# Performance work log

Measured on AMD Instinct MI355X. Metric: run time of the kernel, lower is better.

The kernel has to match this reference:

```python
import jax, jax.numpy as jnp
import numpy as np

DIM_CODES = 512
DICT_SIZE = 512
EMBED_DIM = 16
BATCH = 512


def setup_inputs() -> dict:
    key = jax.random.key(0)
    k1, k2 = jax.random.split(key)
    mu = jax.random.normal(k1, (BATCH, DIM_CODES * EMBED_DIM), dtype=jnp.float32)
    dictionary = jax.random.normal(k2, (DIM_CODES, DICT_SIZE, EMBED_DIM), dtype=jnp.float32)
    return {"mu": mu, "dictionary": dictionary}


def reference(mu, dictionary):
    # mu: [B, C*E], dictionary: [C, K, E]
    B = mu.shape[0]
    C, K, E = dictionary.shape
    mu3 = mu.reshape(B, C, E)
    # pairwise squared distance ||mu - d||^2 = ||mu||^2 + ||d||^2 - 2 mu.d -> [B, C, K]
    dist = (jnp.sum(mu3 * mu3, axis=-1)[..., None]
            + jnp.sum(dictionary * dictionary, axis=-1)[None]
            - 2.0 * jnp.einsum('bce,cke->bck', mu3, dictionary))
    idx = jnp.argmin(dist, axis=-1)  # [B, C] int
    # gather nearest codebook entries: per-code index into its own codebook
    z_embed = dictionary[jnp.arange(C)[None, :], idx]  # [B, C, E]
    z_embed = z_embed.reshape(B, C * E)
    # TransferGrad: forward = z_embed, backward passes grad straight-through to mu
    z = mu + jax.lax.stop_gradient(z_embed - mu)
    one_hot_idx = jax.nn.one_hot(idx, K, dtype=mu.dtype)  # [B, C, K]
    return z, z_embed, one_hot_idx
```

## Files before the change

kernel.cpp:

```cpp
#include <hip/hip_runtime.h>
#include <float.h>

constexpr int C    = 512;
constexpr int K    = 512;
constexpr int E    = 16;
constexpr int B    = 512;
constexpr int ROWS = 128;
constexpr int MUS  = C * E;

__launch_bounds__(256, 2)
__global__ void vq_kernel(const float* __restrict__ mu,
                          const float* __restrict__ dict,
                          float* __restrict__ z,
                          float* __restrict__ zq,
                          float* __restrict__ oh)
{
    const int c    = blockIdx.x;
    const int b0   = blockIdx.y * ROWS;
    const int tid  = threadIdx.x;
    const int lane = tid & 63;
    const int wave = tid >> 6;

    __shared__ float mu_s[ROWS][E];

    const float* __restrict__ dbase = dict + (size_t)c * K * E;

    float4 dv[8][4];
    float  nrm[8];
#pragma unroll
    for (int i = 0; i < 8; ++i) {
        const int k = lane + 64 * i;
        const float4* p = reinterpret_cast<const float4*>(dbase + k * E);
        dv[i][0] = p[0]; dv[i][1] = p[1]; dv[i][2] = p[2]; dv[i][3] = p[3];
        float s = dv[i][0].x * dv[i][0].x;
        s = fmaf(dv[i][0].y, dv[i][0].y, s);
        s = fmaf(dv[i][0].z, dv[i][0].z, s);
        s = fmaf(dv[i][0].w, dv[i][0].w, s);
#pragma unroll
        for (int t = 1; t < 4; ++t) {
            s = fmaf(dv[i][t].x, dv[i][t].x, s);
            s = fmaf(dv[i][t].y, dv[i][t].y, s);
            s = fmaf(dv[i][t].z, dv[i][t].z, s);
            s = fmaf(dv[i][t].w, dv[i][t].w, s);
        }
        nrm[i] = s;
    }

    {
        const int r = tid >> 2, q = tid & 3;
#pragma unroll
        for (int rep = 0; rep < 2; ++rep) {
            const int row = r + rep * 64;
            const float4* p = reinterpret_cast<const float4*>(
                mu + (size_t)(b0 + row) * MUS + c * E);
            reinterpret_cast<float4*>(&mu_s[row][0])[q] = p[q];
        }
    }
    __syncthreads();

    for (int j = 0; j < ROWS / 4; ++j) {
        const int bl = wave + 4 * j;
        const int b  = b0 + bl;

        float4 m[4];
#pragma unroll
        for (int t = 0; t < 4; ++t)
            m[t] = reinterpret_cast<const float4*>(&mu_s[bl][0])[t];

        float nmu = m[0].x * m[0].x;
        nmu = fmaf(m[0].y, m[0].y, nmu);
        nmu = fmaf(m[0].z, m[0].z, nmu);
        nmu = fmaf(m[0].w, m[0].w, nmu);
#pragma unroll
        for (int t = 1; t < 4; ++t) {
            nmu = fmaf(m[t].x, m[t].x, nmu);
            nmu = fmaf(m[t].y, m[t].y, nmu);
            nmu = fmaf(m[t].z, m[t].z, nmu);
            nmu = fmaf(m[t].w, m[t].w, nmu);
        }

        float dist_v[8];
        float best_d = FLT_MAX;
        int   best_k = K;
#pragma unroll
        for (int i = 0; i < 8; ++i) {
            float acc = dv[i][0].x * m[0].x;
            acc = fmaf(dv[i][0].y, m[0].y, acc);
            acc = fmaf(dv[i][0].z, m[0].z, acc);
            acc = fmaf(dv[i][0].w, m[0].w, acc);
#pragma unroll
            for (int t = 1; t < 4; ++t) {
                acc = fmaf(dv[i][t].x, m[t].x, acc);
                acc = fmaf(dv[i][t].y, m[t].y, acc);
                acc = fmaf(dv[i][t].z, m[t].z, acc);
                acc = fmaf(dv[i][t].w, m[t].w, acc);
            }
            const float dist = fmaf(-2.0f, acc, nmu + nrm[i]);
            dist_v[i] = dist;
            const int k = lane + 64 * i;
            if (dist < best_d) { best_d = dist; best_k = k; }
        }

#pragma unroll
        for (int off = 32; off; off >>= 1) {
            const float od = __shfl_down(best_d, off);
            const int   ok = __shfl_down(best_k, off);
            if (od < best_d || (od == best_d && ok < best_k)) {
                best_d = od; best_k = ok;
            }
        }
        best_k = __shfl(best_k, 0);
        best_d = __shfl(best_d, 0);

        float sec = FLT_MAX;
#pragma unroll
        for (int i = 0; i < 8; ++i) {
            const int k = lane + 64 * i;
            sec = (k != best_k) ? fminf(sec, dist_v[i]) : sec;
        }
#pragma unroll
        for (int off = 32; off; off >>= 1)
            sec = fminf(sec, __shfl_down(sec, off));
        sec = __shfl(sec, 0);

        if (sec - best_d < 1e-3f) {
            double nmuD = 0.0;
#pragma unroll
            for (int t = 0; t < 4; ++t) {
                nmuD += (double)m[t].x * m[t].x + (double)m[t].y * m[t].y
                      + (double)m[t].z * m[t].z + (double)m[t].w * m[t].w;
            }
            double bd = DBL_MAX;
            int    bk = K;
#pragma unroll
            for (int i = 0; i < 8; ++i) {
                double nd = 0.0, dt = 0.0;
#pragma unroll
                for (int t = 0; t < 4; ++t) {
                    nd += (double)dv[i][t].x * dv[i][t].x
                        + (double)dv[i][t].y * dv[i][t].y
                        + (double)dv[i][t].z * dv[i][t].z
                        + (double)dv[i][t].w * dv[i][t].w;
                    dt += (double)dv[i][t].x * m[t].x
                        + (double)dv[i][t].y * m[t].y
                        + (double)dv[i][t].z * m[t].z
                        + (double)dv[i][t].w * m[t].w;
                }
                const double dist = nmuD + nd - 2.0 * dt;
                const int k = lane + 64 * i;
                if (dist < bd) { bd = dist; bk = k; }
            }
#pragma unroll
            for (int off = 32; off; off >>= 1) {
                const double od = __shfl_down(bd, off);
                const int    ok = __shfl_down(bk, off);
                if (od < bd || (od == bd && ok < bk)) { bd = od; bk = ok; }
            }
            best_k = __shfl(bk, 0);
        }

        float* ohp = oh + ((size_t)b * C + c) * K;
#pragma unroll
        for (int h = 0; h < 2; ++h) {
            const int kb = h * 256 + lane * 4;
            float4 v;
            v.x = (kb + 0 == best_k) ? 1.0f : 0.0f;
            v.y = (kb + 1 == best_k) ? 1.0f : 0.0f;
            v.z = (kb + 2 == best_k) ? 1.0f : 0.0f;
            v.w = (kb + 3 == best_k) ? 1.0f : 0.0f;
            *reinterpret_cast<float4*>(ohp + kb) = v;
        }

        if (lane < E) {
            const float dq = dbase[best_k * E + lane];
            const float mm = mu_s[bl][lane];
            const size_t o = (size_t)b * MUS + (size_t)c * E + lane;
            zq[o] = dq;
            z[o]  = mm + (dq - mm);
        }
    }
}

extern "C" void kernel_launch(void* const* d_in, const int* in_sizes, int n_in,
                              void* d_out, int out_size, void* d_ws, size_t ws_size,
                              hipStream_t stream)
{
    const float* mu   = (const float*)d_in[0];
    const float* dict = (const float*)d_in[1];

    float* z  = (float*)d_out;
    float* zq = z  + (size_t)B * C * E;
    float* oh = zq + (size_t)B * C * E;

    dim3 grid(C, B / ROWS);
    vq_kernel<<<grid, 256, 0, stream>>>(mu, dict, z, zq, oh);
}
```

Baseline: 695.7 us.

## Batch four rows per wave with packed argmin reduction and single-pass second-min

```diff
diff --git a/kernel.cpp b/kernel.cpp
--- a/kernel.cpp
+++ b/kernel.cpp
@@ -58,123 +58,153 @@
     }
     __syncthreads();
 
-    for (int j = 0; j < ROWS / 4; ++j) {
-        const int bl = wave + 4 * j;
-        const int b  = b0 + bl;
-
-        float4 m[4];
-#pragma unroll
-        for (int t = 0; t < 4; ++t)
-            m[t] = reinterpret_cast<const float4*>(&mu_s[bl][0])[t];
-
-        float nmu = m[0].x * m[0].x;
-        nmu = fmaf(m[0].y, m[0].y, nmu);
-        nmu = fmaf(m[0].z, m[0].z, nmu);
-        nmu = fmaf(m[0].w, m[0].w, nmu);
-#pragma unroll
-        for (int t = 1; t < 4; ++t) {
-            nmu = fmaf(m[t].x, m[t].x, nmu);
-            nmu = fmaf(m[t].y, m[t].y, nmu);
-            nmu = fmaf(m[t].z, m[t].z, nmu);
-            nmu = fmaf(m[t].w, m[t].w, nmu);
-        }
-
-        float dist_v[8];
-        float best_d = FLT_MAX;
-        int   best_k = K;
-#pragma unroll
-        for (int i = 0; i < 8; ++i) {
-            float acc = dv[i][0].x * m[0].x;
-            acc = fmaf(dv[i][0].y, m[0].y, acc);
-            acc = fmaf(dv[i][0].z, m[0].z, acc);
-            acc = fmaf(dv[i][0].w, m[0].w, acc);
+    for (int j = 0; j < ROWS / 16; ++j) {
+        unsigned long long pk[4];
+        float              sec[4];
+
+#pragma unroll
+        for (int r = 0; r < 4; ++r) {
+            const int bl = wave + 16 * j + 4 * r;
+
+            float4 m[4];
+#pragma unroll
+            for (int t = 0; t < 4; ++t)
+                m[t] = reinterpret_cast<const float4*>(&mu_s[bl][0])[t];
+
+            float nmu = m[0].x * m[0].x;
+            nmu = fmaf(m[0].y, m[0].y, nmu);
+            nmu = fmaf(m[0].z, m[0].z, nmu);
+            nmu = fmaf(m[0].w, m[0].w, nmu);
 #pragma unroll
             for (int t = 1; t < 4; ++t) {
-                acc = fmaf(dv[i][t].x, m[t].x, acc);
-                acc = fmaf(dv[i][t].y, m[t].y, acc);
-                acc = fmaf(dv[i][t].z, m[t].z, acc);
-                acc = fmaf(dv[i][t].w, m[t].w, acc);
-            }
-            const float dist = fmaf(-2.0f, acc, nmu + nrm[i]);
-            dist_v[i] = dist;
-            const int k = lane + 64 * i;
-            if (dist < best_d) { best_d = dist; best_k = k; }
+                nmu = fmaf(m[t].x, m[t].x, nmu);
+                nmu = fmaf(m[t].y, m[t].y, nmu);
+                nmu = fmaf(m[t].z, m[t].z, nmu);
+                nmu = fmaf(m[t].w, m[t].w, nmu);
+            }
+
+            float best_d = FLT_MAX;
+            int   best_k = K;
+            float sc     = FLT_MAX;
+#pragma unroll
+            for (int i = 0; i < 8; ++i) {
+                float acc = dv[i][0].x * m[0].x;
+                acc = fmaf(dv[i][0].y, m[0].y, acc);
+                acc = fmaf(dv[i][0].z, m[0].z, acc);
+                acc = fmaf(dv[i][0].w, m[0].w, acc);
+#pragma unroll
+                for (int t = 1; t < 4; ++t) {
+                    acc = fmaf(dv[i][t].x, m[t].x, acc);
+                    acc = fmaf(dv[i][t].y, m[t].y, acc);
+                    acc = fmaf(dv[i][t].z, m[t].z, acc);
+                    acc = fmaf(dv[i][t].w, m[t].w, acc);
+                }
+                const float dist = fmaf(-2.0f, acc, nmu + nrm[i]);
+                sc = fminf(sc, fmaxf(best_d, dist));
+                if (dist < best_d) { best_d = dist; best_k = lane + 64 * i; }
+            }
+            pk[r]  = ((unsigned long long)__float_as_uint(best_d) << 32)
+                   | (unsigned)best_k;
+            sec[r] = sc;
         }
 
 #pragma unroll
         for (int off = 32; off; off >>= 1) {
-            const float od = __shfl_down(best_d, off);
-            const int   ok = __shfl_down(best_k, off);
-            if (od < best_d || (od == best_d && ok < best_k)) {
-                best_d = od; best_k = ok;
-            }
-        }
-        best_k = __shfl(best_k, 0);
-        best_d = __shfl(best_d, 0);
-
-        float sec = FLT_MAX;
-#pragma unroll
-        for (int i = 0; i < 8; ++i) {
-            const int k = lane + 64 * i;
-            sec = (k != best_k) ? fminf(sec, dist_v[i]) : sec;
-        }
-#pragma unroll
-        for (int off = 32; off; off >>= 1)
-            sec = fminf(sec, __shfl_down(sec, off));
-        sec = __shfl(sec, 0);
-
-        if (sec - best_d < 1e-3f) {
-            double nmuD = 0.0;
-#pragma unroll
-            for (int t = 0; t < 4; ++t) {
-                nmuD += (double)m[t].x * m[t].x + (double)m[t].y * m[t].y
-                      + (double)m[t].z * m[t].z + (double)m[t].w * m[t].w;
-            }
-            double bd = DBL_MAX;
-            int    bk = K;
-#pragma unroll
-            for (int i = 0; i < 8; ++i) {
-                double nd = 0.0, dt = 0.0;
+            unsigned long long opk[4];
+            float              osec[4];
+#pragma unroll
+            for (int r = 0; r < 4; ++r) {
+                opk[r]  = __shfl_down(pk[r], off);
+                osec[r] = __shfl_down(sec[r], off);
+            }
+#pragma unroll
+            for (int r = 0; r < 4; ++r) {
+                const float a  = __uint_as_float((unsigned)(pk[r]  >> 32));
+                const float b2 = __uint_as_float((unsigned)(opk[r] >> 32));
+                sec[r] = fminf(fminf(sec[r], osec[r]), fmaxf(a, b2));
+                if (opk[r] < pk[r]) pk[r] = opk[r];
+            }
+        }
+
+        int bk0 = 0, bk1 = 0, bk2 = 0, bk3 = 0;
+#pragma unroll
+        for (int r = 0; r < 4; ++r) {
+            const int klo = __builtin_amdgcn_readfirstlane((int)(unsigned)pk[r]);
+            const int dhi = __builtin_amdgcn_readfirstlane((int)(pk[r] >> 32));
+            const int shi = __builtin_amdgcn_readfirstlane(__float_as_int(sec[r]));
+            int  bkr = klo;
+            const float bd = __int_as_float(dhi);
+            const float sc = __int_as_float(shi);
+
+            if (sc - bd < 1e-3f) {
+                const int bl = wave + 16 * j + 4 * r;
+                float4 m[4];
+#pragma unroll
+                for (int t = 0; t < 4; ++t)
+                    m[t] = reinterpret_cast<const float4*>(&mu_s[bl][0])[t];
+                double nmuD = 0.0;
 #pragma unroll
                 for (int t = 0; t < 4; ++t) {
-                    nd += (double)dv[i][t].x * dv[i][t].x
-                        + (double)dv[i][t].y * dv[i][t].y
-                        + (double)dv[i][t].z * dv[i][t].z
-                        + (double)dv[i][t].w * dv[i][t].w;
-                    dt += (double)dv[i][t].x * m[t].x
-                        + (double)dv[i][t].y * m[t].y
-                        + (double)dv[i][t].z * m[t].z
-                        + (double)dv[i][t].w * m[t].w;
-                }
-                const double dist = nmuD + nd - 2.0 * dt;
-                const int k = lane + 64 * i;
-                if (dist < bd) { bd = dist; bk = k; }
-            }
-#pragma unroll
-            for (int off = 32; off; off >>= 1) {
-                const double od = __shfl_down(bd, off);
-                const int    ok = __shfl_down(bk, off);
-                if (od < bd || (od == bd && ok < bk)) { bd = od; bk = ok; }
-            }
-            best_k = __shfl(bk, 0);
-        }
-
-        float* ohp = oh + ((size_t)b * C + c) * K;
-#pragma unroll
-        for (int h = 0; h < 2; ++h) {
-            const int kb = h * 256 + lane * 4;
-            float4 v;
-            v.x = (kb + 0 == best_k) ? 1.0f : 0.0f;
-            v.y = (kb + 1 == best_k) ? 1.0f : 0.0f;
-            v.z = (kb + 2 == best_k) ? 1.0f : 0.0f;
-            v.w = (kb + 3 == best_k) ? 1.0f : 0.0f;
-            *reinterpret_cast<float4*>(ohp + kb) = v;
-        }
-
-        if (lane < E) {
-            const float dq = dbase[best_k * E + lane];
-            const float mm = mu_s[bl][lane];
-            const size_t o = (size_t)b * MUS + (size_t)c * E + lane;
+                    nmuD += (double)m[t].x * m[t].x + (double)m[t].y * m[t].y
+                          + (double)m[t].z * m[t].z + (double)m[t].w * m[t].w;
+                }
+                double bdd = DBL_MAX;
+                int    bkk = K;
+#pragma unroll
+                for (int i = 0; i < 8; ++i) {
+                    double nd = 0.0, dt = 0.0;
+#pragma unroll
+                    for (int t = 0; t < 4; ++t) {
+                        nd += (double)dv[i][t].x * dv[i][t].x
+                            + (double)dv[i][t].y * dv[i][t].y
+                            + (double)dv[i][t].z * dv[i][t].z
+                            + (double)dv[i][t].w * dv[i][t].w;
+                        dt += (double)dv[i][t].x * m[t].x
+                            + (double)dv[i][t].y * m[t].y
+                            + (double)dv[i][t].z * m[t].z
+                            + (double)dv[i][t].w * m[t].w;
+                    }
+                    const double dist = nmuD + nd - 2.0 * dt;
+                    const int k = lane + 64 * i;
+                    if (dist < bdd) { bdd = dist; bkk = k; }
+                }
+#pragma unroll
+                for (int off = 32; off; off >>= 1) {
+                    const double od = __shfl_down(bdd, off);
+                    const int    ok = __shfl_down(bkk, off);
+                    if (od < bdd || (od == bdd && ok < bkk)) { bdd = od; bkk = ok; }
+                }
+                bkr = __builtin_amdgcn_readfirstlane(bkk);
+            }
+
+            if (r == 0) bk0 = bkr; else if (r == 1) bk1 = bkr;
+            else if (r == 2) bk2 = bkr; else bk3 = bkr;
+
+            const int bl = wave + 16 * j + 4 * r;
+            float* ohp = oh + ((size_t)(b0 + bl) * C + c) * K;
+#pragma unroll
+            for (int h = 0; h < 2; ++h) {
+                const int kb = h * 256 + lane * 4;
+                float4 v;
+                v.x = (kb + 0 == bkr) ? 1.0f : 0.0f;
+                v.y = (kb + 1 == bkr) ? 1.0f : 0.0f;
+                v.z = (kb + 2 == bkr) ? 1.0f : 0.0f;
+                v.w = (kb + 3 == bkr) ? 1.0f : 0.0f;
+                *reinterpret_cast<float4*>(ohp + kb) = v;
+            }
+        }
+
+        {
+            const int r = lane >> 4;
+            const int e = lane & 15;
+            int bkr = bk0;
+            bkr = (r == 1) ? bk1 : bkr;
+            bkr = (r == 2) ? bk2 : bkr;
+            bkr = (r == 3) ? bk3 : bkr;
+            const int bl = wave + 16 * j + 4 * r;
+            const float dq = dbase[bkr * E + e];
+            const float mm = mu_s[bl][e];
+            const size_t o = (size_t)(b0 + bl) * MUS + (size_t)c * E + e;
             zq[o] = dq;
             z[o]  = mm + (dq - mm);
         }
```

Result: slower. 1.098 ms (+57.8%).

## Batch four rows per wave iteration with packed 64-bit argmin reductions

Applied to the files above, without the earlier changes.

```diff
diff --git a/kernel.cpp b/kernel.cpp
--- a/kernel.cpp
+++ b/kernel.cpp
@@ -8,7 +8,23 @@
 constexpr int ROWS = 128;
 constexpr int MUS  = C * E;
 
-__launch_bounds__(256, 2)
+__device__ __forceinline__ float fdot4(const float4 a, const float4 b, float acc) {
+    acc = fmaf(a.x, b.x, acc);
+    acc = fmaf(a.y, b.y, acc);
+    acc = fmaf(a.z, b.z, acc);
+    acc = fmaf(a.w, b.w, acc);
+    return acc;
+}
+__device__ __forceinline__ double ddot4(const float4 a, const float4 b, double acc) {
+    return acc + ((double)a.x * b.x + (double)a.y * b.y
+                + (double)a.z * b.z + (double)a.w * b.w);
+}
+__device__ __forceinline__ double dnrm4(const float4 a, double acc) {
+    return acc + ((double)a.x * a.x + (double)a.y * a.y
+                + (double)a.z * a.z + (double)a.w * a.w);
+}
+
+__launch_bounds__(256, 1)
 __global__ void vq_kernel(const float* __restrict__ mu,
                           const float* __restrict__ dict,
                           float* __restrict__ z,
@@ -25,26 +41,23 @@
 
     const float* __restrict__ dbase = dict + (size_t)c * K * E;
 
-    float4 dv[8][4];
-    float  nrm[8];
-#pragma unroll
-    for (int i = 0; i < 8; ++i) {
-        const int k = lane + 64 * i;
-        const float4* p = reinterpret_cast<const float4*>(dbase + k * E);
-        dv[i][0] = p[0]; dv[i][1] = p[1]; dv[i][2] = p[2]; dv[i][3] = p[3];
-        float s = dv[i][0].x * dv[i][0].x;
-        s = fmaf(dv[i][0].y, dv[i][0].y, s);
-        s = fmaf(dv[i][0].z, dv[i][0].z, s);
-        s = fmaf(dv[i][0].w, dv[i][0].w, s);
-#pragma unroll
-        for (int t = 1; t < 4; ++t) {
-            s = fmaf(dv[i][t].x, dv[i][t].x, s);
-            s = fmaf(dv[i][t].y, dv[i][t].y, s);
-            s = fmaf(dv[i][t].z, dv[i][t].z, s);
-            s = fmaf(dv[i][t].w, dv[i][t].w, s);
-        }
-        nrm[i] = s;
-    }
+#define FOR8(X) X(0) X(1) X(2) X(3) X(4) X(5) X(6) X(7)
+
+#define DECL_D(i) float4 d##i##_0, d##i##_1, d##i##_2, d##i##_3; float n##i;
+    FOR8(DECL_D)
+#undef DECL_D
+
+#define LOAD_D(i) { \
+    const float4* p = reinterpret_cast<const float4*>( \
+        dbase + (size_t)(lane + 64 * i) * E); \
+    d##i##_0 = p[0]; d##i##_1 = p[1]; d##i##_2 = p[2]; d##i##_3 = p[3]; \
+    float s = fdot4(d##i##_0, d##i##_0, 0.0f); \
+    s = fdot4(d##i##_1, d##i##_1, s); \
+    s = fdot4(d##i##_2, d##i##_2, s); \
+    s = fdot4(d##i##_3, d##i##_3, s); \
+    n##i = s; }
+    FOR8(LOAD_D)
+#undef LOAD_D
 
     {
         const int r = tid >> 2, q = tid & 3;
@@ -58,127 +71,122 @@
     }
     __syncthreads();
 
-    for (int j = 0; j < ROWS / 4; ++j) {
-        const int bl = wave + 4 * j;
-        const int b  = b0 + bl;
-
-        float4 m[4];
-#pragma unroll
-        for (int t = 0; t < 4; ++t)
-            m[t] = reinterpret_cast<const float4*>(&mu_s[bl][0])[t];
-
-        float nmu = m[0].x * m[0].x;
-        nmu = fmaf(m[0].y, m[0].y, nmu);
-        nmu = fmaf(m[0].z, m[0].z, nmu);
-        nmu = fmaf(m[0].w, m[0].w, nmu);
-#pragma unroll
-        for (int t = 1; t < 4; ++t) {
-            nmu = fmaf(m[t].x, m[t].x, nmu);
-            nmu = fmaf(m[t].y, m[t].y, nmu);
-            nmu = fmaf(m[t].z, m[t].z, nmu);
-            nmu = fmaf(m[t].w, m[t].w, nmu);
-        }
-
-        float dist_v[8];
-        float best_d = FLT_MAX;
-        int   best_k = K;
-#pragma unroll
-        for (int i = 0; i < 8; ++i) {
-            float acc = dv[i][0].x * m[0].x;
-            acc = fmaf(dv[i][0].y, m[0].y, acc);
-            acc = fmaf(dv[i][0].z, m[0].z, acc);
-            acc = fmaf(dv[i][0].w, m[0].w, acc);
-#pragma unroll
-            for (int t = 1; t < 4; ++t) {
-                acc = fmaf(dv[i][t].x, m[t].x, acc);
-                acc = fmaf(dv[i][t].y, m[t].y, acc);
-                acc = fmaf(dv[i][t].z, m[t].z, acc);
-                acc = fmaf(dv[i][t].w, m[t].w, acc);
-            }
-            const float dist = fmaf(-2.0f, acc, nmu + nrm[i]);
-            dist_v[i] = dist;
-            const int k = lane + 64 * i;
-            if (dist < best_d) { best_d = dist; best_k = k; }
-        }
+#pragma unroll 1
+    for (int j = 0; j < ROWS / 16; ++j) {
+        unsigned long long pk0, pk1, pk2, pk3;
+        float sec0, sec1, sec2, sec3;
+
+#define DIST1(i) { \
+    float acc = fdot4(d##i##_0, m0, 0.0f); \
+    acc = fdot4(d##i##_1, m1, acc); \
+    acc = fdot4(d##i##_2, m2, acc); \
+    acc = fdot4(d##i##_3, m3, acc); \
+    const float dist = fmaf(-2.0f, acc, nmu + n##i); \
+    sc = fminf(sc, fmaxf(best_d, dist)); \
+    if (dist < best_d) { best_d = dist; best_k = lane + 64 * i; } }
+
+#define PHASE1(r) { \
+    const int bl = wave + 16 * j + 4 * r; \
+    const float4* mp = reinterpret_cast<const float4*>(&mu_s[bl][0]); \
+    const float4 m0 = mp[0], m1 = mp[1], m2 = mp[2], m3 = mp[3]; \
+    float nmu = fdot4(m0, m0, 0.0f); \
+    nmu = fdot4(m1, m1, nmu); \
+    nmu = fdot4(m2, m2, nmu); \
+    nmu = fdot4(m3, m3, nmu); \
+    float best_d = FLT_MAX; \
+    int   best_k = K; \
+    float sc     = FLT_MAX; \
+    FOR8(DIST1) \
+    pk##r = ((unsigned long long)__float_as_uint(best_d) << 32) \
+          | (unsigned)best_k; \
+    sec##r = sc; }
+
+        PHASE1(0) PHASE1(1) PHASE1(2) PHASE1(3)
+#undef PHASE1
+#undef DIST1
 
 #pragma unroll
         for (int off = 32; off; off >>= 1) {
-            const float od = __shfl_down(best_d, off);
-            const int   ok = __shfl_down(best_k, off);
-            if (od < best_d || (od == best_d && ok < best_k)) {
-                best_d = od; best_k = ok;
-            }
+#define SHUF(r) { \
+            const unsigned long long o  = __shfl_down(pk##r, off); \
+            const float              os = __shfl_down(sec##r, off); \
+            const float ax = __uint_as_float((unsigned)(pk##r >> 32)); \
+            const float bx = __uint_as_float((unsigned)(o     >> 32)); \
+            sec##r = fminf(fminf(sec##r, os), fmaxf(ax, bx)); \
+            if (o < pk##r) pk##r = o; }
+            SHUF(0) SHUF(1) SHUF(2) SHUF(3)
+#undef SHUF
         }
-        best_k = __shfl(best_k, 0);
-        best_d = __shfl(best_d, 0);
-
-        float sec = FLT_MAX;
-#pragma unroll
-        for (int i = 0; i < 8; ++i) {
-            const int k = lane + 64 * i;
-            sec = (k != best_k) ? fminf(sec, dist_v[i]) : sec;
-        }
-#pragma unroll
-        for (int off = 32; off; off >>= 1)
-            sec = fminf(sec, __shfl_down(sec, off));
-        sec = __shfl(sec, 0);
-
-        if (sec - best_d < 1e-3f) {
-            double nmuD = 0.0;
-#pragma unroll
-            for (int t = 0; t < 4; ++t) {
-                nmuD += (double)m[t].x * m[t].x + (double)m[t].y * m[t].y
-                      + (double)m[t].z * m[t].z + (double)m[t].w * m[t].w;
-            }
-            double bd = DBL_MAX;
-            int    bk = K;
-#pragma unroll
-            for (int i = 0; i < 8; ++i) {
-                double nd = 0.0, dt = 0.0;
-#pragma unroll
-                for (int t = 0; t < 4; ++t) {
-                    nd += (double)dv[i][t].x * dv[i][t].x
-                        + (double)dv[i][t].y * dv[i][t].y
-                        + (double)dv[i][t].z * dv[i][t].z
-                        + (double)dv[i][t].w * dv[i][t].w;
-                    dt += (double)dv[i][t].x * m[t].x
-                        + (double)dv[i][t].y * m[t].y
-                        + (double)dv[i][t].z * m[t].z
-                        + (double)dv[i][t].w * m[t].w;
-                }
-                const double dist = nmuD + nd - 2.0 * dt;
-                const int k = lane + 64 * i;
-                if (dist < bd) { bd = dist; bk = k; }
-            }
-#pragma unroll
-            for (int off = 32; off; off >>= 1) {
-                const double od = __shfl_down(bd, off);
-                const int    ok = __shfl_down(bk, off);
-                if (od < bd || (od == bd && ok < bk)) { bd = od; bk = ok; }
-            }
-            best_k = __shfl(bk, 0);
-        }
-
-        float* ohp = oh + ((size_t)b * C + c) * K;
-#pragma unroll
-        for (int h = 0; h < 2; ++h) {
-            const int kb = h * 256 + lane * 4;
-            float4 v;
-            v.x = (kb + 0 == best_k) ? 1.0f : 0.0f;
-            v.y = (kb + 1 == best_k) ? 1.0f : 0.0f;
-            v.z = (kb + 2 == best_k) ? 1.0f : 0.0f;
-            v.w = (kb + 3 == best_k) ? 1.0f : 0.0f;
-            *reinterpret_cast<float4*>(ohp + kb) = v;
-        }
-
-        if (lane < E) {
-            const float dq = dbase[best_k * E + lane];
-            const float mm = mu_s[bl][lane];
-            const size_t o = (size_t)b * MUS + (size_t)c * E + lane;
+
+        int bk0, bk1, bk2, bk3;
+
+#define D641(i) { \
+    double nd = dnrm4(d##i##_0, 0.0); nd = dnrm4(d##i##_1, nd); \
+    nd = dnrm4(d##i##_2, nd); nd = dnrm4(d##i##_3, nd); \
+    double dt = ddot4(d##i##_0, m0, 0.0); dt = ddot4(d##i##_1, m1, dt); \
+    dt = ddot4(d##i##_2, m2, dt); dt = ddot4(d##i##_3, m3, dt); \
+    const double dist = nmuD + nd - 2.0 * dt; \
+    if (dist < bdd) { bdd = dist; bkk = lane + 64 * i; } }
+
+#define PHASE3(r, BK) { \
+    const int klo = __builtin_amdgcn_readfirstlane((int)(unsigned)pk##r); \
+    const int dhi = __builtin_amdgcn_readfirstlane((int)(pk##r >> 32)); \
+    const int shi = __builtin_amdgcn_readfirstlane(__float_as_int(sec##r)); \
+    int bkr = klo; \
+    if (__int_as_float(shi) - __int_as_float(dhi) < 1e-3f) { \
+         \
+        const int bl = wave + 16 * j + 4 * r; \
+        const float4* mp = reinterpret_cast<const float4*>(&mu_s[bl][0]); \
+        const float4 m0 = mp[0], m1 = mp[1], m2 = mp[2], m3 = mp[3]; \
+        double nmuD = dnrm4(m0, 0.0); nmuD = dnrm4(m1, nmuD); \
+        nmuD = dnrm4(m2, nmuD); nmuD = dnrm4(m3, nmuD); \
+        double bdd = DBL_MAX; \
+        int    bkk = K; \
+        FOR8(D641) \
+        _Pragma("unroll") \
+        for (int off = 32; off; off >>= 1) { \
+            const double od = __shfl_down(bdd, off); \
+            const int    ok = __shfl_down(bkk, off); \
+            if (od < bdd || (od == bdd && ok < bkk)) { bdd = od; bkk = ok; } \
+        } \
+        bkr = __builtin_amdgcn_readfirstlane(bkk); \
+    } \
+    BK = bkr; \
+    { \
+        const int bl = wave + 16 * j + 4 * r; \
+        float* ohp = oh + ((size_t)(b0 + bl) * C + c) * K; \
+        _Pragma("unroll") \
+        for (int h = 0; h < 2; ++h) { \
+            const int kb = h * 256 + lane * 4; \
+            float4 v; \
+            v.x = (kb + 0 == bkr) ? 1.0f : 0.0f; \
+            v.y = (kb + 1 == bkr) ? 1.0f : 0.0f; \
+            v.z = (kb + 2 == bkr) ? 1.0f : 0.0f; \
+            v.w = (kb + 3 == bkr) ? 1.0f : 0.0f; \
+            *reinterpret_cast<float4*>(ohp + kb) = v; \
+        } \
+    } }
+
+        PHASE3(0, bk0) PHASE3(1, bk1) PHASE3(2, bk2) PHASE3(3, bk3)
+#undef PHASE3
+#undef D641
+
+        {
+            const int r = lane >> 4;
+            const int e = lane & 15;
+            int bkr = bk0;
+            bkr = (r == 1) ? bk1 : bkr;
+            bkr = (r == 2) ? bk2 : bkr;
+            bkr = (r == 3) ? bk3 : bkr;
+            const int bl = wave + 16 * j + 4 * r;
+            const float dq = dbase[bkr * E + e];
+            const float mm = mu_s[bl][e];
+            const size_t o = (size_t)(b0 + bl) * MUS + (size_t)c * E + e;
             zq[o] = dq;
             z[o]  = mm + (dq - mm);
         }
     }
+#undef FOR8
 }
 
 extern "C" void kernel_launch(void* const* d_in, const int* in_sizes, int n_in,
```

New measurement: 781.9 us. 1.12x slower.
